# Performance work log

Hardware: AMD Instinct MI355X
Metric: run time of the kernel (lower is better)

Reference implementation:

```python
import jax, jax.numpy as jnp
import numpy as np

M_SQRT1_2 = 0.7071067811865476
P_DROP = 0.1  # activation_dropout


def setup_inputs() -> dict:
    key = jax.random.key(0)
    k1, k2, k3, k4 = jax.random.split(key, 4)
    N, FFN, EMB = 8192, 4096, 1024
    x = jax.random.normal(k1, (N, FFN), dtype=jnp.float16)
    weight = (jax.random.normal(k2, (EMB, FFN), dtype=jnp.float32) * (1.0 / np.sqrt(FFN))).astype(jnp.float16)
    bias = jax.random.normal(k3, (EMB,), dtype=jnp.float16)
    mask = jax.random.uniform(k4, (N, FFN)) >= P_DROP  # keep mask (bool)
    return {"x": x, "weight": weight, "bias": bias, "mask": mask}


def reference(x, weight, bias, mask):
    # GELU computed in fp32, cast back to fp16 (matches the custom IR)
    xf = x.astype(jnp.float32)
    g = (0.5 * xf * (1.0 + jax.lax.erf(xf * M_SQRT1_2))).astype(jnp.float16)
    # dropout: mask then scale by 1/(1-p) in fp16
    scale = jnp.float16(1.0 / (1.0 - P_DROP))
    h = g * mask.astype(jnp.float16) * scale  # [N, FFN]
    # y[N0, N2] = sum_N1 h[N0, N1] * weight[N2, N1] + bias[N2]
    y = jnp.einsum('nf,ef->ne', h, weight) + bias[None, :]
    return y
```

## Files before the change

### kernel.cpp

```cpp
#include <hip/hip_runtime.h>
#include <stdint.h>

typedef uint32_t u32;
typedef uint16_t u16;

static constexpr int M_DIM = 8192;
static constexpr int N_DIM = 1024;
static constexpr int K_DIM = 4096;

static constexpr size_t FRAG_U16 = 512;
static constexpr size_t WT_BYTES = 64ull * 128 * FRAG_U16 * 2;
static constexpr size_t WS_NEEDED = WT_BYTES;

typedef __attribute__((ext_vector_type(8))) _Float16 half8;
typedef __attribute__((ext_vector_type(4))) float f32x4;

__device__ __forceinline__ u32 pack2(float a, float b) {
  union { _Float16 h[2]; u32 u; } p;
  p.h[0] = (_Float16)a;
  p.h[1] = (_Float16)b;
  return p.u;
}

__device__ __forceinline__ float gelu_drop(float x, u32 keep) {
  float ax = fabsf(x);
  float z  = ax * 0.70710678f;
  float t  = __builtin_amdgcn_rcpf(fmaf(0.3275911f, z, 1.0f));
  float poly = fmaf(fmaf(fmaf(fmaf(1.061405429f, t, -1.453152027f),
                              t, 1.421413741f),
                         t, -0.284496736f),
                    t, 0.254829592f) * t;
  float e   = exp2f(z * z * -1.44269504f);
  float erf = fmaf(-poly, e, 1.0f);
  float g   = 0.5f * x * (1.0f + copysignf(erf, x));
  return keep ? g * 1.1111112f : 0.0f;
}

static constexpr int W_PAIRS = 64 * 64;
static constexpr int WPACK_BLOCKS = W_PAIRS / 4;

__global__ __launch_bounds__(256)
void wpack_kernel(const float* __restrict__ W, u16* __restrict__ Wt) {
  const int l     = threadIdx.x & 63;
  const int pj    = blockIdx.x * 4 + (threadIdx.x >> 6);
  const int row16 = l & 15;
  const int kof   = (l >> 4) << 4;
  const int fsub  = kof >> 5;
  const int q0    = (kof & 31) >> 3;

  const int nb = pj >> 6, kp = pj & 63;
  const float* wp = W + (size_t)(nb * 16 + row16) * K_DIM + kp * 64 + kof;
  float4 w0 = *(const float4*)(wp + 0);
  float4 w1 = *(const float4*)(wp + 4);
  float4 w2 = *(const float4*)(wp + 8);
  float4 w3 = *(const float4*)(wp + 12);
  const int f = kp * 2 + fsub;
  u16* dst = Wt + (size_t)(nb * 128 + f) * FRAG_U16 + (size_t)(row16 + 16 * q0) * 8;
  *(uint4*)(dst)       = make_uint4(pack2(w0.x, w0.y), pack2(w0.z, w0.w),
                                    pack2(w1.x, w1.y), pack2(w1.z, w1.w));
  *(uint4*)(dst + 128) = make_uint4(pack2(w2.x, w2.y), pack2(w2.z, w2.w),
                                    pack2(w3.x, w3.y), pack2(w3.z, w3.w));
}

__global__ __launch_bounds__(512, 1)
void fused_gemm_kernel(const float* __restrict__ X, const int* __restrict__ Mask,
                       const u16* __restrict__ Wt, const float* __restrict__ Bias,
                       float* __restrict__ Out) {
  __shared__ __attribute__((aligned(16))) u16 Abuf[2][4096];

  const int tid  = threadIdx.x;
  const int lane = tid & 63;
  const int wv   = tid >> 6;
  const int m0   = blockIdx.x * 32;

  const int xrow = tid >> 4;
  const int xe   = tid & 15;
  const float* Xp = X    + (size_t)(m0 + xrow) * K_DIM + xe * 8;
  const int*   Mp = Mask + (size_t)(m0 + xrow) * K_DIM + xe * 8;
  float4 xs0, xs1;
  uint4  ms0, ms1;
  auto loadX = [&](int c) {
    const float* xp = Xp + c * 128;
    const int*   mp = Mp + c * 128;
    xs0 = *(const float4*)(xp);
    xs1 = *(const float4*)(xp + 4);
    ms0 = *(const uint4*)(mp);
    ms1 = *(const uint4*)(mp + 4);
  };
  const u32 aOff = (u32)((((xe >> 2) * 2 + (xrow >> 4)) * 1024) +
                         ((xe & 3) * 256) + ((xrow & 15) * 16));
  auto writeA = [&](int buf) {
    u32 o0 = pack2(gelu_drop(xs0.x, ms0.x), gelu_drop(xs0.y, ms0.y));
    u32 o1 = pack2(gelu_drop(xs0.z, ms0.z), gelu_drop(xs0.w, ms0.w));
    u32 o2 = pack2(gelu_drop(xs1.x, ms1.x), gelu_drop(xs1.y, ms1.y));
    u32 o3 = pack2(gelu_drop(xs1.z, ms1.z), gelu_drop(xs1.w, ms1.w));
    *(uint4*)((char*)Abuf[buf] + aOff) = make_uint4(o0, o1, o2, o3);
  };

  const char* WtB = (const char*)Wt;
  const size_t bBase = (size_t)(wv * 8) * 131072 + (size_t)lane * 16;
  half8 bs0[8], bs1[8];
  auto loadB = [&](int kt, half8 (&bs)[8]) {
#pragma unroll
    for (int j = 0; j < 8; ++j)
      bs[j] = *(const half8*)(WtB + bBase + (size_t)j * 131072 + (size_t)kt * 1024);
  };

  f32x4 acc[2][8];
#pragma unroll
  for (int i = 0; i < 2; ++i)
#pragma unroll
    for (int j = 0; j < 8; ++j)
      acc[i][j] = (f32x4){0.f, 0.f, 0.f, 0.f};

  auto step = [&](int ab, int ktl, half8 (&bs)[8]) {
    half8 ar[2];
#pragma unroll
    for (int rf = 0; rf < 2; ++rf)
      ar[rf] = *(const half8*)((const char*)Abuf[ab] +
                               (size_t)((ktl * 2 + rf) * 1024 + lane * 16));
    __builtin_amdgcn_s_setprio(1);
#pragma unroll
    for (int rf = 0; rf < 2; ++rf)
#pragma unroll
      for (int j = 0; j < 8; ++j)
        acc[rf][j] = __builtin_amdgcn_mfma_f32_16x16x32_f16(ar[rf], bs[j], acc[rf][j], 0, 0, 0);
    __builtin_amdgcn_s_setprio(0);
  };

  loadX(0);
  writeA(0);
  loadX(1);
  loadB(0, bs0);
  loadB(1, bs1);
  asm volatile("s_waitcnt lgkmcnt(0)" ::: "memory");
  __builtin_amdgcn_s_barrier();

#pragma unroll 1
  for (int c = 0; c < 32; ++c) {
    const int ab = c & 1;
    const int kt0 = c * 4;
    if (c + 1 < 32) writeA(ab ^ 1);
    if (c + 2 < 32) loadX(c + 2);
    step(ab, 0, bs0);
    if (kt0 + 2 < 128) loadB(kt0 + 2, bs0);
    step(ab, 1, bs1);
    if (kt0 + 3 < 128) loadB(kt0 + 3, bs1);
    step(ab, 2, bs0);
    if (kt0 + 4 < 128) loadB(kt0 + 4, bs0);
    step(ab, 3, bs1);
    if (kt0 + 5 < 128) loadB(kt0 + 5, bs1);
    if (c + 1 < 32) {
      asm volatile("s_waitcnt lgkmcnt(0)" ::: "memory");
      __builtin_amdgcn_s_barrier();
    }
  }

  const int fr = lane & 15;
  const int rq = (lane >> 4) << 2;
#pragma unroll
  for (int rf = 0; rf < 2; ++rf) {
    const int row0 = m0 + rf * 16 + rq;
#pragma unroll
    for (int j = 0; j < 8; ++j) {
      const int col = (wv * 8 + j) * 16 + fr;
      const float b = Bias[col];
#pragma unroll
      for (int r = 0; r < 4; ++r)
        Out[(size_t)(row0 + r) * N_DIM + col] = acc[rf][j][r] + b;
    }
  }
}

static constexpr int A_STRIDE = 40;

__global__ __launch_bounds__(256, 2)
void fused_fallback_kernel(const float* __restrict__ X, const float* __restrict__ W,
                           const float* __restrict__ Bias, const int* __restrict__ Mask,
                           float* __restrict__ Out) {
  __shared__ __attribute__((aligned(16))) _Float16 As[128 * A_STRIDE];
  __shared__ __attribute__((aligned(16))) _Float16 Bs[128 * 32];

  const int tid  = threadIdx.x;
  const int lane = tid & 63;
  const int wv   = tid >> 6;
  const int wr   = wv >> 1;
  const int wc   = wv & 1;
  const int bm = blockIdx.x & 63;
  const int bn = blockIdx.x >> 6;
  const int m0 = bm * 128;
  const int n0 = bn * 128;

  const int a_m = tid >> 1;
  const int a_k = (tid & 1) << 4;
  const float* xptr = X    + (size_t)(m0 + a_m) * K_DIM + a_k;
  const int*   mptr = Mask + (size_t)(m0 + a_m) * K_DIM + a_k;
  _Float16* a_lds = &As[a_m * A_STRIDE + a_k];

  const int i0 = tid, i1 = tid + 256;
  const float* wp0 = W + (size_t)(n0 + (i0 >> 2)) * K_DIM + ((i0 & 3) << 3);
  const float* wp1 = W + (size_t)(n0 + (i1 >> 2)) * K_DIM + ((i1 & 3) << 3);
  _Float16* bl0 = &Bs[i0 * 8];
  _Float16* bl1 = &Bs[i1 * 8];

  f32x4 acc[4][4];
#pragma unroll
  for (int i = 0; i < 4; ++i)
#pragma unroll
    for (int j = 0; j < 4; ++j)
      acc[i][j] = (f32x4){0.f, 0.f, 0.f, 0.f};

  float4 xf0 = *(const float4*)(xptr +  0);
  float4 xf1 = *(const float4*)(xptr +  4);
  float4 xf2 = *(const float4*)(xptr +  8);
  float4 xf3 = *(const float4*)(xptr + 12);
  uint4  mr0 = *(const uint4*)(mptr +  0);
  uint4  mr1 = *(const uint4*)(mptr +  4);
  uint4  mr2 = *(const uint4*)(mptr +  8);
  uint4  mr3 = *(const uint4*)(mptr + 12);
  float4 wf0 = *(const float4*)(wp0 + 0);
  float4 wf1 = *(const float4*)(wp0 + 4);
  float4 wf2 = *(const float4*)(wp1 + 0);
  float4 wf3 = *(const float4*)(wp1 + 4);

#pragma unroll 1
  for (int kt = 0; kt < 128; ++kt) {
    {
      float xs[16] = {xf0.x, xf0.y, xf0.z, xf0.w, xf1.x, xf1.y, xf1.z, xf1.w,
                      xf2.x, xf2.y, xf2.z, xf2.w, xf3.x, xf3.y, xf3.z, xf3.w};
      u32 mk[16]   = {mr0.x, mr0.y, mr0.z, mr0.w, mr1.x, mr1.y, mr1.z, mr1.w,
                      mr2.x, mr2.y, mr2.z, mr2.w, mr3.x, mr3.y, mr3.z, mr3.w};
      u32 ow[8];
#pragma unroll
      for (int e = 0; e < 8; ++e)
        ow[e] = pack2(gelu_drop(xs[2 * e], mk[2 * e]), gelu_drop(xs[2 * e + 1], mk[2 * e + 1]));
      ((uint4*)a_lds)[0] = make_uint4(ow[0], ow[1], ow[2], ow[3]);
      ((uint4*)a_lds)[1] = make_uint4(ow[4], ow[5], ow[6], ow[7]);
    }
    {
      *(uint4*)bl0 = make_uint4(pack2(wf0.x, wf0.y), pack2(wf0.z, wf0.w),
                                pack2(wf1.x, wf1.y), pack2(wf1.z, wf1.w));
      *(uint4*)bl1 = make_uint4(pack2(wf2.x, wf2.y), pack2(wf2.z, wf2.w),
                                pack2(wf3.x, wf3.y), pack2(wf3.z, wf3.w));
    }
    __syncthreads();

    if (kt + 1 < 128) {
      xptr += 32; mptr += 32; wp0 += 32; wp1 += 32;
      xf0 = *(const float4*)(xptr +  0);
      xf1 = *(const float4*)(xptr +  4);
      xf2 = *(const float4*)(xptr +  8);
      xf3 = *(const float4*)(xptr + 12);
      mr0 = *(const uint4*)(mptr +  0);
      mr1 = *(const uint4*)(mptr +  4);
      mr2 = *(const uint4*)(mptr +  8);
      mr3 = *(const uint4*)(mptr + 12);
      wf0 = *(const float4*)(wp0 + 0);
      wf1 = *(const float4*)(wp0 + 4);
      wf2 = *(const float4*)(wp1 + 0);
      wf3 = *(const float4*)(wp1 + 4);
    }

    {
      const int fr2 = lane & 15;
      const int fk2 = (lane >> 4) << 3;
      half8 ar[4], br[4];
#pragma unroll
      for (int i = 0; i < 4; ++i)
        ar[i] = *(const half8*)&As[(wr * 64 + i * 16 + fr2) * A_STRIDE + fk2];
#pragma unroll
      for (int j = 0; j < 4; ++j)
        br[j] = *(const half8*)&Bs[(wc * 64 + j * 16 + fr2) * 32 + fk2];
#pragma unroll
      for (int i = 0; i < 4; ++i)
#pragma unroll
        for (int j = 0; j < 4; ++j)
          acc[i][j] = __builtin_amdgcn_mfma_f32_16x16x32_f16(ar[i], br[j], acc[i][j], 0, 0, 0);
    }
    __syncthreads();
  }

  const int fr = lane & 15;
  const int rq = (lane >> 4) << 2;
  float bv[4];
#pragma unroll
  for (int j = 0; j < 4; ++j)
    bv[j] = Bias[n0 + wc * 64 + j * 16 + fr];
#pragma unroll
  for (int i = 0; i < 4; ++i) {
    const int row0 = m0 + wr * 64 + i * 16 + rq;
#pragma unroll
    for (int j = 0; j < 4; ++j) {
      const int col = n0 + wc * 64 + j * 16 + fr;
#pragma unroll
      for (int r = 0; r < 4; ++r)
        Out[(size_t)(row0 + r) * N_DIM + col] = acc[i][j][r] + bv[j];
    }
  }
}

extern "C" void kernel_launch(void* const* d_in, const int* in_sizes, int n_in,
                              void* d_out, int out_size, void* d_ws, size_t ws_size,
                              hipStream_t stream) {
  const float* X    = (const float*)d_in[0];
  const float* W    = (const float*)d_in[1];
  const float* Bias = (const float*)d_in[2];
  const int*   Mk   = (const int*)d_in[3];
  float* Out = (float*)d_out;

  if (ws_size >= WS_NEEDED) {
    u16* Wt = (u16*)d_ws;
    wpack_kernel<<<WPACK_BLOCKS, 256, 0, stream>>>(W, Wt);
    fused_gemm_kernel<<<M_DIM / 32, 512, 0, stream>>>(X, Mk, Wt, Bias, Out);
  } else {
    fused_fallback_kernel<<<64 * 8, 256, 0, stream>>>(X, W, Bias, Mk, Out);
  }
}
```

Baseline: 381.4 us.

## Retile fused GEMM to 64x512 blocks with XCD-aware block mapping

Changes each block from a 32x1024 output tile to a 64x512 tile, with 8 waves arranged 2x4 so each wave still computes 32x128. Block IDs are remapped so that blocks on the same XCD (bid&7) share one N half, which is meant to improve L2 reuse of the packed weights. The intent is to halve redundant X/mask reads per output and to balance weight versus activation traffic. The grid drops from 256... actually stays 256 blocks, and the A-tile shared buffer doubles. Each block now computes GELU for twice as many rows, but each X row is processed by two blocks.

```diff
diff --git a/kernel.cpp b/kernel.cpp
--- a/kernel.cpp
+++ b/kernel.cpp
@@ -66,39 +66,57 @@
 void fused_gemm_kernel(const float* __restrict__ X, const int* __restrict__ Mask,
                        const u16* __restrict__ Wt, const float* __restrict__ Bias,
                        float* __restrict__ Out) {
-  __shared__ __attribute__((aligned(16))) u16 Abuf[2][4096];
+  __shared__ __attribute__((aligned(16))) u16 Abuf[2][8192];
 
   const int tid  = threadIdx.x;
   const int lane = tid & 63;
   const int wv   = tid >> 6;
-  const int m0   = blockIdx.x * 32;
-
-  const int xrow = tid >> 4;
-  const int xe   = tid & 15;
-  const float* Xp = X    + (size_t)(m0 + xrow) * K_DIM + xe * 8;
-  const int*   Mp = Mask + (size_t)(m0 + xrow) * K_DIM + xe * 8;
-  float4 xs0, xs1;
-  uint4  ms0, ms1;
+  const int wr   = wv >> 2;
+  const int wc   = wv & 3;
+
+  const int bid = blockIdx.x;
+  const int xcd = bid & 7;
+  const int jh  = xcd >> 2;
+  const int it  = (xcd & 3) * 32 + (bid >> 3);
+  const int m0  = it * 64;
+  const int n0  = jh * 512;
+
+  const int xrow = tid >> 3;
+  const int xe   = tid & 7;
+  const float* Xp = X    + (size_t)(m0 + xrow) * K_DIM + xe * 16;
+  const int*   Mp = Mask + (size_t)(m0 + xrow) * K_DIM + xe * 16;
+  float4 xs0, xs1, xs2, xs3;
+  uint4  ms0, ms1, ms2, ms3;
   auto loadX = [&](int c) {
     const float* xp = Xp + c * 128;
     const int*   mp = Mp + c * 128;
-    xs0 = *(const float4*)(xp);
+    xs0 = *(const float4*)(xp + 0);
     xs1 = *(const float4*)(xp + 4);
-    ms0 = *(const uint4*)(mp);
+    xs2 = *(const float4*)(xp + 8);
+    xs3 = *(const float4*)(xp + 12);
+    ms0 = *(const uint4*)(mp + 0);
     ms1 = *(const uint4*)(mp + 4);
+    ms2 = *(const uint4*)(mp + 8);
+    ms3 = *(const uint4*)(mp + 12);
   };
-  const u32 aOff = (u32)((((xe >> 2) * 2 + (xrow >> 4)) * 1024) +
-                         ((xe & 3) * 256) + ((xrow & 15) * 16));
+  const u32 aOff = (u32)((((xe >> 1) * 4 + (xrow >> 4)) * 1024) +
+                         ((xe & 1) * 2) * 256 + ((xrow & 15) * 16));
   auto writeA = [&](int buf) {
     u32 o0 = pack2(gelu_drop(xs0.x, ms0.x), gelu_drop(xs0.y, ms0.y));
     u32 o1 = pack2(gelu_drop(xs0.z, ms0.z), gelu_drop(xs0.w, ms0.w));
     u32 o2 = pack2(gelu_drop(xs1.x, ms1.x), gelu_drop(xs1.y, ms1.y));
     u32 o3 = pack2(gelu_drop(xs1.z, ms1.z), gelu_drop(xs1.w, ms1.w));
-    *(uint4*)((char*)Abuf[buf] + aOff) = make_uint4(o0, o1, o2, o3);
+    u32 o4 = pack2(gelu_drop(xs2.x, ms2.x), gelu_drop(xs2.y, ms2.y));
+    u32 o5 = pack2(gelu_drop(xs2.z, ms2.z), gelu_drop(xs2.w, ms2.w));
+    u32 o6 = pack2(gelu_drop(xs3.x, ms3.x), gelu_drop(xs3.y, ms3.y));
+    u32 o7 = pack2(gelu_drop(xs3.z, ms3.z), gelu_drop(xs3.w, ms3.w));
+    char* base = (char*)Abuf[buf] + aOff;
+    *(uint4*)(base)       = make_uint4(o0, o1, o2, o3);
+    *(uint4*)(base + 256) = make_uint4(o4, o5, o6, o7);
   };
 
   const char* WtB = (const char*)Wt;
-  const size_t bBase = (size_t)(wv * 8) * 131072 + (size_t)lane * 16;
+  const size_t bBase = (size_t)(jh * 32 + wc * 8) * 131072 + (size_t)lane * 16;
   half8 bs0[8], bs1[8];
   auto loadB = [&](int kt, half8 (&bs)[8]) {
 #pragma unroll
@@ -118,7 +136,7 @@
 #pragma unroll
     for (int rf = 0; rf < 2; ++rf)
       ar[rf] = *(const half8*)((const char*)Abuf[ab] +
-                               (size_t)((ktl * 2 + rf) * 1024 + lane * 16));
+                               (size_t)(((ktl * 4 + wr * 2 + rf) * 1024) + lane * 16));
     __builtin_amdgcn_s_setprio(1);
 #pragma unroll
     for (int rf = 0; rf < 2; ++rf)
@@ -160,10 +178,10 @@
   const int rq = (lane >> 4) << 2;
 #pragma unroll
   for (int rf = 0; rf < 2; ++rf) {
-    const int row0 = m0 + rf * 16 + rq;
+    const int row0 = m0 + wr * 32 + rf * 16 + rq;
 #pragma unroll
     for (int j = 0; j < 8; ++j) {
-      const int col = (wv * 8 + j) * 16 + fr;
+      const int col = n0 + wc * 128 + j * 16 + fr;
       const float b = Bias[col];
 #pragma unroll
       for (int r = 0; r < 4; ++r)
@@ -311,7 +329,7 @@
   if (ws_size >= WS_NEEDED) {
     u16* Wt = (u16*)d_ws;
     wpack_kernel<<<WPACK_BLOCKS, 256, 0, stream>>>(W, Wt);
-    fused_gemm_kernel<<<M_DIM / 32, 512, 0, stream>>>(X, Mk, Wt, Bias, Out);
+    fused_gemm_kernel<<<256, 512, 0, stream>>>(X, Mk, Wt, Bias, Out);
   } else {
     fused_fallback_kernel<<<64 * 8, 256, 0, stream>>>(X, W, Bias, Mk, Out);
   }
```

Result: slower. 399.3 us (+4.7%).
